# Kernel tuning notes

Hardware: AMD Instinct MI355X
Metric: run time of the kernel (lower is better)

The kernel has to match this reference:

```python
import jax, jax.numpy as jnp
import numpy as np

N = 100000
E = 1600000
D_IN, D_H, D_OUT = 128, 128, 64


def sage_conv(x, src, dst, Wl, bl, Wr, n_nodes):
    # PyG SAGEConv (aggr='mean', root_weight=True):
    # out_i = Wl @ mean_{j->i} x_j + bl + Wr @ x_i
    msg_sum = jax.ops.segment_sum(x[src], dst, num_segments=n_nodes)  # [N, d]
    deg = jax.ops.segment_sum(jnp.ones((src.shape[0],), x.dtype), dst, num_segments=n_nodes)
    agg = msg_sum / jnp.maximum(deg, 1.0)[:, None]
    return agg @ Wl + bl + x @ Wr


def setup_inputs() -> dict:
    key = jax.random.key(0)
    ks = jax.random.split(key, 12)
    x = jax.random.normal(ks[0], (N, D_IN), dtype=jnp.float32)
    edge_index = jax.random.randint(ks[1], (2, E), 0, N, dtype=jnp.int32)
    s1 = 1.0 / np.sqrt(D_IN)
    s2 = 1.0 / np.sqrt(D_H)
    return {
        "x": x,
        "edge_index": edge_index,
        "Wl1": jax.random.uniform(ks[2], (D_IN, D_H), jnp.float32, -s1, s1),
        "bl1": jax.random.uniform(ks[3], (D_H,), jnp.float32, -s1, s1),
        "Wr1": jax.random.uniform(ks[4], (D_IN, D_H), jnp.float32, -s1, s1),
        "Wl2": jax.random.uniform(ks[5], (D_H, D_H), jnp.float32, -s2, s2),
        "bl2": jax.random.uniform(ks[6], (D_H,), jnp.float32, -s2, s2),
        "Wr2": jax.random.uniform(ks[7], (D_H, D_H), jnp.float32, -s2, s2),
        "Wl3": jax.random.uniform(ks[8], (D_H, D_OUT), jnp.float32, -s2, s2),
        "bl3": jax.random.uniform(ks[9], (D_OUT,), jnp.float32, -s2, s2),
        "Wr3": jax.random.uniform(ks[10], (D_H, D_OUT), jnp.float32, -s2, s2),
    }


def reference(x, edge_index, Wl1, bl1, Wr1, Wl2, bl2, Wr2, Wl3, bl3, Wr3):
    src, dst = edge_index[0], edge_index[1]
    n = x.shape[0]
    # conv_first + relu (dropout is identity in eval mode)
    h = jax.nn.relu(sage_conv(x, src, dst, Wl1, bl1, Wr1, n))
    # conv_hidden + relu (layer_num=3 -> one hidden layer)
    h = jax.nn.relu(sage_conv(h, src, dst, Wl2, bl2, Wr2, n))
    # conv_out + L2 normalize (F.normalize, eps=1e-12)
    h = sage_conv(h, src, dst, Wl3, bl3, Wr3, n)
    norm = jnp.maximum(jnp.linalg.norm(h, axis=-1, keepdims=True), 1e-12)
    return h / norm
```

## Files before the change

kernel.cpp:

```cpp
#include <hip/hip_runtime.h>


#define BSHIFT 9
#define BNODES (1 << BSHIFT)
#define ROUND_LOG 12

typedef __attribute__((ext_vector_type(8))) short bf16x8;
typedef __attribute__((ext_vector_type(4))) float f32x4;
typedef __attribute__((ext_vector_type(8))) unsigned short u16x8;

__device__ inline float bf2f(unsigned short u) {
  unsigned v = ((unsigned)u) << 16;
  return __builtin_bit_cast(float, v);
}
__device__ inline unsigned short f2bf(float f) {
  unsigned u = __builtin_bit_cast(unsigned, f);
  u += 0x7FFF + ((u >> 16) & 1);
  return (unsigned short)(u >> 16);
}


__global__ __launch_bounds__(256) void cast_x_kernel(
    const float* __restrict__ in, unsigned short* __restrict__ out, int n8) {
  for (int i = blockIdx.x * 256 + threadIdx.x; i < n8; i += gridDim.x * 256) {
    float4 a = *(const float4*)(in + (size_t)i * 8);
    float4 b = *(const float4*)(in + (size_t)i * 8 + 4);
    u16x8 o;
    o[0] = f2bf(a.x); o[1] = f2bf(a.y); o[2] = f2bf(a.z); o[3] = f2bf(a.w);
    o[4] = f2bf(b.x); o[5] = f2bf(b.y); o[6] = f2bf(b.z); o[7] = f2bf(b.w);
    *(u16x8*)(out + (size_t)i * 8) = o;
  }
}

__global__ __launch_bounds__(256) void wtcast_kernel(
    const float* __restrict__ W, unsigned short* __restrict__ WT, int K,
    int M) {
  for (int i = blockIdx.x * 256 + threadIdx.x; i < K * M;
       i += gridDim.x * 256) {
    int k = i / M, m = i - k * M;
    WT[(size_t)m * K + k] = f2bf(W[i]);
  }
}


__global__ __launch_bounds__(256) void hist_kernel(const int* __restrict__ dst,
                                                   int E,
                                                   int* __restrict__ gcnt) {
  __shared__ int h[256];
  h[threadIdx.x] = 0;
  __syncthreads();
  for (int i = blockIdx.x * 256 + threadIdx.x; i < E; i += gridDim.x * 256)
    atomicAdd(&h[dst[i] >> BSHIFT], 1);
  __syncthreads();
  int v = h[threadIdx.x];
  if (v) atomicAdd(&gcnt[threadIdx.x], v);
}

__global__ __launch_bounds__(256) void bucket_scan_kernel(
    const int* __restrict__ gcnt, int NB, int* __restrict__ gbase,
    int* __restrict__ gcur, int* __restrict__ row_ptr, int N, int E) {
  __shared__ int sh[256];
  const int t = threadIdx.x;
  const int v = (t < NB) ? gcnt[t] : 0;
  sh[t] = v;
  __syncthreads();
  for (int d = 1; d < 256; d <<= 1) {
    int u = (t >= d) ? sh[t - d] : 0;
    __syncthreads();
    sh[t] += u;
    __syncthreads();
  }
  gbase[t] = sh[t] - v;
  gcur[t] = sh[t] - v;
  if (t == 0) row_ptr[N] = E;
}

__global__ __launch_bounds__(256) void partition_kernel(
    const int* __restrict__ src, const int* __restrict__ dst, int E,
    int* __restrict__ gcur, unsigned int* __restrict__ pairs) {
  __shared__ int lcnt[256];
  __shared__ int lbase[256];
  const int t = threadIdx.x;
  const int nRounds = (E + (1 << ROUND_LOG) - 1) >> ROUND_LOG;
  for (int r = blockIdx.x; r < nRounds; r += gridDim.x) {
    const int base = r << ROUND_LOG;
    lcnt[t] = 0;
    __syncthreads();
    int pk[16];
#pragma unroll
    for (int j = 0; j < 16; ++j) {
      int idx = base + j * 256 + t;
      pk[j] = -1;
      if (idx < E) {
        int b = dst[idx] >> BSHIFT;
        int lp = atomicAdd(&lcnt[b], 1);
        pk[j] = (b << 12) | lp;
      }
    }
    __syncthreads();
    int c = lcnt[t];
    if (c > 0) lbase[t] = atomicAdd(&gcur[t], c);
    __syncthreads();
#pragma unroll
    for (int j = 0; j < 16; ++j) {
      if (pk[j] >= 0) {
        int idx = base + j * 256 + t;
        int b = pk[j] >> 12;
        int p = lbase[b] + (pk[j] & 0xFFF);
        pairs[p] = ((unsigned)(dst[idx] & (BNODES - 1)) << 17) |
                   (unsigned)src[idx];
      }
    }
    __syncthreads();
  }
}

__global__ __launch_bounds__(256) void bucket_csr_kernel(
    const unsigned int* __restrict__ pairs, const int* __restrict__ gbase,
    const int* __restrict__ gcnt, int N, int* __restrict__ row_ptr,
    int* __restrict__ csr) {
  const int b = blockIdx.x;
  const int t = threadIdx.x;
  const int nb0 = b << BSHIFT;
  __shared__ int ldeg[BNODES];
  __shared__ int lscan[256];
  __shared__ int lcur[BNODES];
  const int base = gbase[b];
  const int cnt = gcnt[b];
  ldeg[t] = 0;
  ldeg[t + 256] = 0;
  __syncthreads();
  for (int e = t; e < cnt; e += 256)
    atomicAdd(&ldeg[pairs[base + e] >> 17], 1);
  __syncthreads();
  const int s2 = ldeg[2 * t] + ldeg[2 * t + 1];
  lscan[t] = s2;
  __syncthreads();
  for (int d = 1; d < 256; d <<= 1) {
    int u = (t >= d) ? lscan[t - d] : 0;
    __syncthreads();
    lscan[t] += u;
    __syncthreads();
  }
  const int ex = lscan[t] - s2;
  const int o0 = base + ex;
  const int o1 = o0 + ldeg[2 * t];
  const int n0 = nb0 + 2 * t;
  if (n0 < N) row_ptr[n0] = o0;
  if (n0 + 1 < N) row_ptr[n0 + 1] = o1;
  lcur[2 * t] = o0;
  lcur[2 * t + 1] = o1;
  __syncthreads();
  for (int e = t; e < cnt; e += 256) {
    unsigned int p = pairs[base + e];
    int pos = atomicAdd(&lcur[p >> 17], 1);
    csr[pos] = (int)(p & 0x1FFFF);
  }
}


__global__ __launch_bounds__(256) void gemm_dual_bf16(
    const unsigned short* __restrict__ A, const unsigned short* __restrict__ BT1,
    const unsigned short* __restrict__ BT2, const float* __restrict__ bias,
    unsigned short* __restrict__ C1, unsigned short* __restrict__ C2, int N,
    int M) {
  __shared__ unsigned short As[128][72];
  __shared__ unsigned short Bs[64][72];
  const int t = threadIdx.x;
  const int half = gridDim.x >> 1;
  int bx = blockIdx.x;
  const unsigned short* BT;
  unsigned short* C;
  const float* bs;
  if (bx < half) {
    BT = BT1; C = C1; bs = nullptr;
  } else {
    BT = BT2; C = C2; bs = bias; bx -= half;
  }
  const int rb = blockIdx.y * 128;
  const int cb = bx * 64;
  const int l = t & 63, wv = t >> 6;
  const int wr = wv >> 1, wc = wv & 1;
  const int lr = l & 15, kb = l >> 4;

  f32x4 acc[4][2];
#pragma unroll
  for (int fr = 0; fr < 4; ++fr)
#pragma unroll
    for (int fc = 0; fc < 2; ++fc) acc[fr][fc] = (f32x4)(0.f);

  const int sr = t >> 3;
  const int sc = (t & 7) * 8;

  for (int kt = 0; kt < 128; kt += 64) {
#pragma unroll
    for (int i = 0; i < 4; ++i) {
      int r = i * 32 + sr;
      int grow = rb + r;
      uint4 v = make_uint4(0, 0, 0, 0);
      if (grow < N) v = *(const uint4*)(A + (size_t)grow * 128 + kt + sc);
      *(uint4*)&As[r][sc] = v;
    }
#pragma unroll
    for (int i = 0; i < 2; ++i) {
      int r = i * 32 + sr;
      uint4 v = *(const uint4*)(BT + (size_t)(cb + r) * 128 + kt + sc);
      *(uint4*)&Bs[r][sc] = v;
    }
    __syncthreads();
#pragma unroll
    for (int ks = 0; ks < 2; ++ks) {
      bf16x8 a[4], b[2];
#pragma unroll
      for (int fr = 0; fr < 4; ++fr)
        a[fr] = *(const bf16x8*)&As[wr * 64 + fr * 16 + lr][ks * 32 + kb * 8];
#pragma unroll
      for (int fc = 0; fc < 2; ++fc)
        b[fc] = *(const bf16x8*)&Bs[wc * 32 + fc * 16 + lr][ks * 32 + kb * 8];
#pragma unroll
      for (int fr = 0; fr < 4; ++fr)
#pragma unroll
        for (int fc = 0; fc < 2; ++fc)
          acc[fr][fc] = __builtin_amdgcn_mfma_f32_16x16x32_bf16(
              a[fr], b[fc], acc[fr][fc], 0, 0, 0);
    }
    __syncthreads();
  }
#pragma unroll
  for (int fc = 0; fc < 2; ++fc) {
    int col = cb + wc * 32 + fc * 16 + lr;
    float bv = bs ? bs[col] : 0.f;
#pragma unroll
    for (int fr = 0; fr < 4; ++fr) {
      int row0 = rb + wr * 64 + fr * 16 + kb * 4;
#pragma unroll
      for (int j = 0; j < 4; ++j) {
        int row = row0 + j;
        if (row < N) C[(size_t)row * M + col] = f2bf(acc[fr][fc][j] + bv);
      }
    }
  }
}


__global__ __launch_bounds__(256) void agg_relu_bf16_128(
    const unsigned short* __restrict__ z, const unsigned short* __restrict__ w,
    const int* __restrict__ row_ptr, const int* __restrict__ csr,
    unsigned short* __restrict__ out, int N) {
  const int g = threadIdx.x >> 4;
  const int lane = threadIdx.x & 15;
  const int node = blockIdx.x * 16 + g;
  if (node >= N) return;
  const int s = row_ptr[node];
  const int e = row_ptr[node + 1];
  float a0[8] = {0, 0, 0, 0, 0, 0, 0, 0};
  float a1[8] = {0, 0, 0, 0, 0, 0, 0, 0};
  int i = s;
  for (; i + 1 < e; i += 2) {
    u16x8 v0 = *(const u16x8*)(z + (size_t)csr[i] * 128 + lane * 8);
    u16x8 v1 = *(const u16x8*)(z + (size_t)csr[i + 1] * 128 + lane * 8);
#pragma unroll
    for (int j = 0; j < 8; ++j) {
      a0[j] += bf2f(v0[j]);
      a1[j] += bf2f(v1[j]);
    }
  }
  if (i < e) {
    u16x8 v0 = *(const u16x8*)(z + (size_t)csr[i] * 128 + lane * 8);
#pragma unroll
    for (int j = 0; j < 8; ++j) a0[j] += bf2f(v0[j]);
  }
  const int d = e - s;
  const float inv = 1.0f / (float)(d > 0 ? d : 1);
  u16x8 wv = *(const u16x8*)(w + (size_t)node * 128 + lane * 8);
  u16x8 o;
#pragma unroll
  for (int j = 0; j < 8; ++j)
    o[j] = f2bf(fmaxf(fmaf(a0[j] + a1[j], inv, bf2f(wv[j])), 0.f));
  *(u16x8*)(out + (size_t)node * 128 + lane * 8) = o;
}

__global__ __launch_bounds__(256) void agg_norm_bf16_64(
    const unsigned short* __restrict__ z, const unsigned short* __restrict__ w,
    const int* __restrict__ row_ptr, const int* __restrict__ csr,
    float* __restrict__ out, int N) {
  const int g = threadIdx.x >> 3;
  const int lane = threadIdx.x & 7;
  const int node = blockIdx.x * 32 + g;
  if (node >= N) return;
  const int s = row_ptr[node];
  const int e = row_ptr[node + 1];
  float a0[8] = {0, 0, 0, 0, 0, 0, 0, 0};
  float a1[8] = {0, 0, 0, 0, 0, 0, 0, 0};
  int i = s;
  for (; i + 1 < e; i += 2) {
    u16x8 v0 = *(const u16x8*)(z + (size_t)csr[i] * 64 + lane * 8);
    u16x8 v1 = *(const u16x8*)(z + (size_t)csr[i + 1] * 64 + lane * 8);
#pragma unroll
    for (int j = 0; j < 8; ++j) {
      a0[j] += bf2f(v0[j]);
      a1[j] += bf2f(v1[j]);
    }
  }
  if (i < e) {
    u16x8 v0 = *(const u16x8*)(z + (size_t)csr[i] * 64 + lane * 8);
#pragma unroll
    for (int j = 0; j < 8; ++j) a0[j] += bf2f(v0[j]);
  }
  const int d = e - s;
  const float inv = 1.0f / (float)(d > 0 ? d : 1);
  u16x8 wv = *(const u16x8*)(w + (size_t)node * 64 + lane * 8);
  float v[8];
  float n2 = 0.f;
#pragma unroll
  for (int j = 0; j < 8; ++j) {
    v[j] = fmaf(a0[j] + a1[j], inv, bf2f(wv[j]));
    n2 = fmaf(v[j], v[j], n2);
  }
  n2 += __shfl_xor(n2, 1);
  n2 += __shfl_xor(n2, 2);
  n2 += __shfl_xor(n2, 4);
  const float invn = 1.0f / fmaxf(sqrtf(n2), 1e-12f);
  float* op = out + (size_t)node * 64 + lane * 8;
  float4 o0 = make_float4(v[0] * invn, v[1] * invn, v[2] * invn, v[3] * invn);
  float4 o1 = make_float4(v[4] * invn, v[5] * invn, v[6] * invn, v[7] * invn);
  *(float4*)op = o0;
  *(float4*)(op + 4) = o1;
}


extern "C" void kernel_launch(void* const* d_in, const int* in_sizes, int n_in,
                              void* d_out, int out_size, void* d_ws,
                              size_t ws_size, hipStream_t stream) {
  const float* x   = (const float*)d_in[0];
  const int*   ei  = (const int*)d_in[1];
  const float* Wl1 = (const float*)d_in[2];
  const float* bl1 = (const float*)d_in[3];
  const float* Wr1 = (const float*)d_in[4];
  const float* Wl2 = (const float*)d_in[5];
  const float* bl2 = (const float*)d_in[6];
  const float* Wr2 = (const float*)d_in[7];
  const float* Wl3 = (const float*)d_in[8];
  const float* bl3 = (const float*)d_in[9];
  const float* Wr3 = (const float*)d_in[10];

  const int N = in_sizes[0] / 128;
  const int E = in_sizes[1] / 2;
  const int* src = ei;
  const int* dst = ei + E;
  const int NB = (N + BNODES - 1) >> BSHIFT;

  char* ws = (char*)d_ws;
  size_t off = 0;
  auto take = [&](size_t bytes) -> char* {
    char* p = ws + off;
    off += (bytes + 255) & ~(size_t)255;
    return p;
  };
  unsigned short* xb   = (unsigned short*)take((size_t)N * 128 * 2);
  unsigned short* h    = (unsigned short*)take((size_t)N * 128 * 2);
  unsigned short* z    = (unsigned short*)take((size_t)N * 128 * 2);
  unsigned short* w    = (unsigned short*)take((size_t)N * 128 * 2);
  unsigned short* WT[6];
  for (int i = 0; i < 6; ++i) WT[i] = (unsigned short*)take(128 * 128 * 2);
  int*          row_ptr = (int*)take((size_t)(N + 1) * 4);
  int*          csr     = (int*)take((size_t)E * 4);
  unsigned int* pairs   = (unsigned int*)take((size_t)E * 4);
  int*          gcnt    = (int*)take(256 * 4);
  int*          gbase   = (int*)take(256 * 4);
  int*          gcur    = (int*)take(256 * 4);
  (void)ws_size;

  hipMemsetAsync(gcnt, 0, 256 * 4, stream);
  hist_kernel<<<1024, 256, 0, stream>>>(dst, E, gcnt);
  bucket_scan_kernel<<<1, 256, 0, stream>>>(gcnt, NB, gbase, gcur, row_ptr, N, E);
  const int nRounds = (E + (1 << ROUND_LOG) - 1) >> ROUND_LOG;
  partition_kernel<<<nRounds, 256, 0, stream>>>(src, dst, E, gcur, pairs);
  bucket_csr_kernel<<<NB, 256, 0, stream>>>(pairs, gbase, gcnt, N, row_ptr, csr);

  cast_x_kernel<<<2048, 256, 0, stream>>>(x, xb, N * 16);
  wtcast_kernel<<<64, 256, 0, stream>>>(Wl1, WT[0], 128, 128);
  wtcast_kernel<<<64, 256, 0, stream>>>(Wr1, WT[1], 128, 128);
  wtcast_kernel<<<64, 256, 0, stream>>>(Wl2, WT[2], 128, 128);
  wtcast_kernel<<<64, 256, 0, stream>>>(Wr2, WT[3], 128, 128);
  wtcast_kernel<<<32, 256, 0, stream>>>(Wl3, WT[4], 128, 64);
  wtcast_kernel<<<32, 256, 0, stream>>>(Wr3, WT[5], 128, 64);

  const dim3 blk(256);
  const int rowBlocks = (N + 127) / 128;
  const dim3 gd2(4, rowBlocks);
  const dim3 gd1(2, rowBlocks);
  const int aggB128 = (N + 15) / 16;
  const int aggB64  = (N + 31) / 32;

  gemm_dual_bf16<<<gd2, blk, 0, stream>>>(xb, WT[0], WT[1], bl1, z, w, N, 128);
  agg_relu_bf16_128<<<aggB128, blk, 0, stream>>>(z, w, row_ptr, csr, h, N);
  gemm_dual_bf16<<<gd2, blk, 0, stream>>>(h, WT[2], WT[3], bl2, z, w, N, 128);
  agg_relu_bf16_128<<<aggB128, blk, 0, stream>>>(z, w, row_ptr, csr, h, N);
  gemm_dual_bf16<<<gd1, blk, 0, stream>>>(h, WT[4], WT[5], bl3, z, w, N, 64);
  agg_norm_bf16_64<<<aggB64, blk, 0, stream>>>(z, w, row_ptr, csr,
                                               (float*)d_out, N);
}
```

Measured before the change: 458.2 us.

## Slice Z/W into 16-column feature planes for cache-friendly gather aggregation

The first two layers' GEMM outputs are written in a sliced layout: eight planes of 16 columns each. The aggregation kernel then handles one slice per block, so each gather of a neighbour row touches 32 bytes, and the per-slice working set (N×32B) can stay in L2 across edges. The dual GEMM now computes both Wl and Wr products in a single block, with both weight matrices loaded as one concatenated B tile, and weight casting is merged into three launches. In exchange, each gather uses smaller 8-byte loads, the edge list is re-read once per slice, and the GEMM stores become scattered.

```diff
diff --git a/kernel.cpp b/kernel.cpp
--- a/kernel.cpp
+++ b/kernel.cpp
@@ -32,13 +32,15 @@
   }
 }
 
-__global__ __launch_bounds__(256) void wtcast_kernel(
-    const float* __restrict__ W, unsigned short* __restrict__ WT, int K,
-    int M) {
-  for (int i = blockIdx.x * 256 + threadIdx.x; i < K * M;
+__global__ __launch_bounds__(256) void wtcast2_kernel(
+    const float* __restrict__ Wl, const float* __restrict__ Wr,
+    unsigned short* __restrict__ BT, int K, int M) {
+  const int total = 2 * M * K;
+  for (int i = blockIdx.x * 256 + threadIdx.x; i < total;
        i += gridDim.x * 256) {
-    int k = i / M, m = i - k * M;
-    WT[(size_t)m * K + k] = f2bf(W[i]);
+    int r = i / K, k = i - r * K;
+    float v = (r < M) ? Wl[(size_t)k * M + r] : Wr[(size_t)k * M + (r - M)];
+    BT[i] = f2bf(v);
   }
 }
 
@@ -159,35 +161,26 @@
 }
 
 
-__global__ __launch_bounds__(256) void gemm_dual_bf16(
-    const unsigned short* __restrict__ A, const unsigned short* __restrict__ BT1,
-    const unsigned short* __restrict__ BT2, const float* __restrict__ bias,
-    unsigned short* __restrict__ C1, unsigned short* __restrict__ C2, int N,
-    int M) {
+template <int MH, bool SLICED>
+__global__ __launch_bounds__(256) void gemm_dual(
+    const unsigned short* __restrict__ A, const unsigned short* __restrict__ BT,
+    const float* __restrict__ bias, unsigned short* __restrict__ Zs,
+    unsigned short* __restrict__ Ws, int N) {
+  constexpr int MT = 2 * MH;
+  constexpr int F = MH / 16;
   __shared__ unsigned short As[128][72];
-  __shared__ unsigned short Bs[64][72];
+  __shared__ unsigned short Bs[MT][72];
   const int t = threadIdx.x;
-  const int half = gridDim.x >> 1;
-  int bx = blockIdx.x;
-  const unsigned short* BT;
-  unsigned short* C;
-  const float* bs;
-  if (bx < half) {
-    BT = BT1; C = C1; bs = nullptr;
-  } else {
-    BT = BT2; C = C2; bs = bias; bx -= half;
-  }
-  const int rb = blockIdx.y * 128;
-  const int cb = bx * 64;
+  const int rb = blockIdx.x * 128;
   const int l = t & 63, wv = t >> 6;
   const int wr = wv >> 1, wc = wv & 1;
   const int lr = l & 15, kb = l >> 4;
 
-  f32x4 acc[4][2];
+  f32x4 acc[4][F];
 #pragma unroll
   for (int fr = 0; fr < 4; ++fr)
 #pragma unroll
-    for (int fc = 0; fc < 2; ++fc) acc[fr][fc] = (f32x4)(0.f);
+    for (int fc = 0; fc < F; ++fc) acc[fr][fc] = (f32x4)(0.f);
 
   const int sr = t >> 3;
   const int sc = (t & 7) * 8;
@@ -202,83 +195,100 @@
       *(uint4*)&As[r][sc] = v;
     }
 #pragma unroll
-    for (int i = 0; i < 2; ++i) {
+    for (int i = 0; i < MT / 32; ++i) {
       int r = i * 32 + sr;
-      uint4 v = *(const uint4*)(BT + (size_t)(cb + r) * 128 + kt + sc);
+      uint4 v = *(const uint4*)(BT + (size_t)r * 128 + kt + sc);
       *(uint4*)&Bs[r][sc] = v;
     }
     __syncthreads();
 #pragma unroll
     for (int ks = 0; ks < 2; ++ks) {
-      bf16x8 a[4], b[2];
+      bf16x8 a[4], b[F];
 #pragma unroll
       for (int fr = 0; fr < 4; ++fr)
         a[fr] = *(const bf16x8*)&As[wr * 64 + fr * 16 + lr][ks * 32 + kb * 8];
 #pragma unroll
-      for (int fc = 0; fc < 2; ++fc)
-        b[fc] = *(const bf16x8*)&Bs[wc * 32 + fc * 16 + lr][ks * 32 + kb * 8];
+      for (int fc = 0; fc < F; ++fc)
+        b[fc] = *(const bf16x8*)&Bs[wc * MH + fc * 16 + lr][ks * 32 + kb * 8];
 #pragma unroll
       for (int fr = 0; fr < 4; ++fr)
 #pragma unroll
-        for (int fc = 0; fc < 2; ++fc)
+        for (int fc = 0; fc < F; ++fc)
           acc[fr][fc] = __builtin_amdgcn_mfma_f32_16x16x32_bf16(
               a[fr], b[fc], acc[fr][fc], 0, 0, 0);
     }
     __syncthreads();
   }
-#pragma unroll
-  for (int fc = 0; fc < 2; ++fc) {
-    int col = cb + wc * 32 + fc * 16 + lr;
-    float bv = bs ? bs[col] : 0.f;
+  unsigned short* Cb = wc ? Ws : Zs;
+#pragma unroll
+  for (int fc = 0; fc < F; ++fc) {
+    const int cm = fc * 16 + lr;
+    const float bv = wc ? bias[cm] : 0.f;
 #pragma unroll
     for (int fr = 0; fr < 4; ++fr) {
-      int row0 = rb + wr * 64 + fr * 16 + kb * 4;
+      const int row0 = rb + wr * 64 + fr * 16 + kb * 4;
 #pragma unroll
       for (int j = 0; j < 4; ++j) {
-        int row = row0 + j;
-        if (row < N) C[(size_t)row * M + col] = f2bf(acc[fr][fc][j] + bv);
+        const int row = row0 + j;
+        if (row < N) {
+          size_t idx = SLICED ? ((size_t)(fc * N + row) * 16 + lr)
+                              : ((size_t)row * MH + cm);
+          Cb[idx] = f2bf(acc[fr][fc][j] + bv);
+        }
       }
     }
   }
 }
 
 
-__global__ __launch_bounds__(256) void agg_relu_bf16_128(
-    const unsigned short* __restrict__ z, const unsigned short* __restrict__ w,
+__global__ __launch_bounds__(256) void agg_relu_sliced(
+    const unsigned short* __restrict__ Zs, const unsigned short* __restrict__ Ws,
     const int* __restrict__ row_ptr, const int* __restrict__ csr,
     unsigned short* __restrict__ out, int N) {
-  const int g = threadIdx.x >> 4;
-  const int lane = threadIdx.x & 15;
-  const int node = blockIdx.x * 16 + g;
+  const int s = blockIdx.x & 7;
+  const int grp = blockIdx.x >> 3;
+  const int node = grp * 64 + (threadIdx.x >> 2);
+  const int l4 = threadIdx.x & 3;
   if (node >= N) return;
-  const int s = row_ptr[node];
+  const int sB = row_ptr[node];
   const int e = row_ptr[node + 1];
-  float a0[8] = {0, 0, 0, 0, 0, 0, 0, 0};
-  float a1[8] = {0, 0, 0, 0, 0, 0, 0, 0};
-  int i = s;
+  const unsigned short* zb = Zs + (size_t)s * N * 16 + l4 * 4;
+  float a0[4] = {0, 0, 0, 0}, a1[4] = {0, 0, 0, 0};
+  int i = sB;
   for (; i + 1 < e; i += 2) {
-    u16x8 v0 = *(const u16x8*)(z + (size_t)csr[i] * 128 + lane * 8);
-    u16x8 v1 = *(const u16x8*)(z + (size_t)csr[i + 1] * 128 + lane * 8);
-#pragma unroll
-    for (int j = 0; j < 8; ++j) {
-      a0[j] += bf2f(v0[j]);
-      a1[j] += bf2f(v1[j]);
-    }
+    uint2 v0 = *(const uint2*)(zb + (size_t)csr[i] * 16);
+    uint2 v1 = *(const uint2*)(zb + (size_t)csr[i + 1] * 16);
+    a0[0] += bf2f((unsigned short)v0.x);
+    a0[1] += bf2f((unsigned short)(v0.x >> 16));
+    a0[2] += bf2f((unsigned short)v0.y);
+    a0[3] += bf2f((unsigned short)(v0.y >> 16));
+    a1[0] += bf2f((unsigned short)v1.x);
+    a1[1] += bf2f((unsigned short)(v1.x >> 16));
+    a1[2] += bf2f((unsigned short)v1.y);
+    a1[3] += bf2f((unsigned short)(v1.y >> 16));
   }
   if (i < e) {
-    u16x8 v0 = *(const u16x8*)(z + (size_t)csr[i] * 128 + lane * 8);
-#pragma unroll
-    for (int j = 0; j < 8; ++j) a0[j] += bf2f(v0[j]);
-  }
-  const int d = e - s;
+    uint2 v0 = *(const uint2*)(zb + (size_t)csr[i] * 16);
+    a0[0] += bf2f((unsigned short)v0.x);
+    a0[1] += bf2f((unsigned short)(v0.x >> 16));
+    a0[2] += bf2f((unsigned short)v0.y);
+    a0[3] += bf2f((unsigned short)(v0.y >> 16));
+  }
+  const int d = e - sB;
   const float inv = 1.0f / (float)(d > 0 ? d : 1);
-  u16x8 wv = *(const u16x8*)(w + (size_t)node * 128 + lane * 8);
-  u16x8 o;
-#pragma unroll
-  for (int j = 0; j < 8; ++j)
-    o[j] = f2bf(fmaxf(fmaf(a0[j] + a1[j], inv, bf2f(wv[j])), 0.f));
-  *(u16x8*)(out + (size_t)node * 128 + lane * 8) = o;
-}
+  uint2 wv = *(const uint2*)(Ws + ((size_t)s * N + node) * 16 + l4 * 4);
+  float r0 = fmaxf(fmaf(a0[0] + a1[0], inv, bf2f((unsigned short)wv.x)), 0.f);
+  float r1 =
+      fmaxf(fmaf(a0[1] + a1[1], inv, bf2f((unsigned short)(wv.x >> 16))), 0.f);
+  float r2 = fmaxf(fmaf(a0[2] + a1[2], inv, bf2f((unsigned short)wv.y)), 0.f);
+  float r3 =
+      fmaxf(fmaf(a0[3] + a1[3], inv, bf2f((unsigned short)(wv.y >> 16))), 0.f);
+  uint2 o;
+  o.x = (unsigned)f2bf(r0) | ((unsigned)f2bf(r1) << 16);
+  o.y = (unsigned)f2bf(r2) | ((unsigned)f2bf(r3) << 16);
+  *(uint2*)(out + (size_t)node * 128 + s * 16 + l4 * 4) = o;
+}
+
 
 __global__ __launch_bounds__(256) void agg_norm_bf16_64(
     const unsigned short* __restrict__ z, const unsigned short* __restrict__ w,
@@ -361,8 +371,9 @@
   unsigned short* h    = (unsigned short*)take((size_t)N * 128 * 2);
   unsigned short* z    = (unsigned short*)take((size_t)N * 128 * 2);
   unsigned short* w    = (unsigned short*)take((size_t)N * 128 * 2);
-  unsigned short* WT[6];
-  for (int i = 0; i < 6; ++i) WT[i] = (unsigned short*)take(128 * 128 * 2);
+  unsigned short* BT1  = (unsigned short*)take(256 * 128 * 2);
+  unsigned short* BT2  = (unsigned short*)take(256 * 128 * 2);
+  unsigned short* BT3  = (unsigned short*)take(128 * 128 * 2);
   int*          row_ptr = (int*)take((size_t)(N + 1) * 4);
   int*          csr     = (int*)take((size_t)E * 4);
   unsigned int* pairs   = (unsigned int*)take((size_t)E * 4);
@@ -379,25 +390,20 @@
   bucket_csr_kernel<<<NB, 256, 0, stream>>>(pairs, gbase, gcnt, N, row_ptr, csr);
 
   cast_x_kernel<<<2048, 256, 0, stream>>>(x, xb, N * 16);
-  wtcast_kernel<<<64, 256, 0, stream>>>(Wl1, WT[0], 128, 128);
-  wtcast_kernel<<<64, 256, 0, stream>>>(Wr1, WT[1], 128, 128);
-  wtcast_kernel<<<64, 256, 0, stream>>>(Wl2, WT[2], 128, 128);
-  wtcast_kernel<<<64, 256, 0, stream>>>(Wr2, WT[3], 128, 128);
-  wtcast_kernel<<<32, 256, 0, stream>>>(Wl3, WT[4], 128, 64);
-  wtcast_kernel<<<32, 256, 0, stream>>>(Wr3, WT[5], 128, 64);
+  wtcast2_kernel<<<128, 256, 0, stream>>>(Wl1, Wr1, BT1, 128, 128);
+  wtcast2_kernel<<<128, 256, 0, stream>>>(Wl2, Wr2, BT2, 128, 128);
+  wtcast2_kernel<<<64, 256, 0, stream>>>(Wl3, Wr3, BT3, 128, 64);
 
   const dim3 blk(256);
   const int rowBlocks = (N + 127) / 128;
-  const dim3 gd2(4, rowBlocks);
-  const dim3 gd1(2, rowBlocks);
-  const int aggB128 = (N + 15) / 16;
-  const int aggB64  = (N + 31) / 32;
-
-  gemm_dual_bf16<<<gd2, blk, 0, stream>>>(xb, WT[0], WT[1], bl1, z, w, N, 128);
-  agg_relu_bf16_128<<<aggB128, blk, 0, stream>>>(z, w, row_ptr, csr, h, N);
-  gemm_dual_bf16<<<gd2, blk, 0, stream>>>(h, WT[2], WT[3], bl2, z, w, N, 128);
-  agg_relu_bf16_128<<<aggB128, blk, 0, stream>>>(z, w, row_ptr, csr, h, N);
-  gemm_dual_bf16<<<gd1, blk, 0, stream>>>(h, WT[4], WT[5], bl3, z, w, N, 64);
+  const int aggSliced = ((N + 63) / 64) * 8;
+  const int aggB64 = (N + 31) / 32;
+
+  gemm_dual<128, true><<<rowBlocks, blk, 0, stream>>>(xb, BT1, bl1, z, w, N);
+  agg_relu_sliced<<<aggSliced, blk, 0, stream>>>(z, w, row_ptr, csr, h, N);
+  gemm_dual<128, true><<<rowBlocks, blk, 0, stream>>>(h, BT2, bl2, z, w, N);
+  agg_relu_sliced<<<aggSliced, blk, 0, stream>>>(z, w, row_ptr, csr, h, N);
+  gemm_dual<64, false><<<rowBlocks, blk, 0, stream>>>(h, BT3, bl3, z, w, N);
   agg_norm_bf16_64<<<aggB64, blk, 0, stream>>>(z, w, row_ptr, csr,
                                                (float*)d_out, N);
 }
```

Result: slower. 620.4 us (+35.4%).

## Fuse x cast into first GEMM, merge weight casts, widen GEMM tiles, unroll gather

Applied to the files above, without the earlier changes.

The first layer's GEMM now reads fp32 x directly and converts it to bf16 while staging into shared memory, which removes the separate cast kernel and its bf16 round trip through memory. The six weight-transpose kernels become one launch that packs the Wl and Wr weights of each layer into a single stacked buffer. Each GEMM block now covers the full output width (128 or 64 columns), so the A tile is loaded once per matrix instead of twice, at the cost of more accumulator registers. The 128-wide aggregation loop is unrolled by four with independent accumulators to keep more gathers in flight.

```diff
diff --git a/kernel.cpp b/kernel.cpp
--- a/kernel.cpp
+++ b/kernel.cpp
@@ -20,25 +20,31 @@
 }
 
 
-__global__ __launch_bounds__(256) void cast_x_kernel(
-    const float* __restrict__ in, unsigned short* __restrict__ out, int n8) {
-  for (int i = blockIdx.x * 256 + threadIdx.x; i < n8; i += gridDim.x * 256) {
-    float4 a = *(const float4*)(in + (size_t)i * 8);
-    float4 b = *(const float4*)(in + (size_t)i * 8 + 4);
-    u16x8 o;
-    o[0] = f2bf(a.x); o[1] = f2bf(a.y); o[2] = f2bf(a.z); o[3] = f2bf(a.w);
-    o[4] = f2bf(b.x); o[5] = f2bf(b.y); o[6] = f2bf(b.z); o[7] = f2bf(b.w);
-    *(u16x8*)(out + (size_t)i * 8) = o;
-  }
-}
-
-__global__ __launch_bounds__(256) void wtcast_kernel(
-    const float* __restrict__ W, unsigned short* __restrict__ WT, int K,
-    int M) {
-  for (int i = blockIdx.x * 256 + threadIdx.x; i < K * M;
+__global__ __launch_bounds__(256) void wtcast_all_kernel(
+    const float* __restrict__ Wl1, const float* __restrict__ Wr1,
+    const float* __restrict__ Wl2, const float* __restrict__ Wr2,
+    const float* __restrict__ Wl3, const float* __restrict__ Wr3,
+    unsigned short* __restrict__ BT1, unsigned short* __restrict__ BT2,
+    unsigned short* __restrict__ BT3) {
+  const int K = 128;
+  const int n12 = 2 * 128 * K;
+  const int n3 = 2 * 64 * K;
+  const int total = 2 * n12 + n3;
+  for (int i = blockIdx.x * 256 + threadIdx.x; i < total;
        i += gridDim.x * 256) {
-    int k = i / M, m = i - k * M;
-    WT[(size_t)m * K + k] = f2bf(W[i]);
+    const float *Wl, *Wr;
+    unsigned short* BT;
+    int j, M;
+    if (i < n12) {
+      Wl = Wl1; Wr = Wr1; BT = BT1; j = i; M = 128;
+    } else if (i < 2 * n12) {
+      Wl = Wl2; Wr = Wr2; BT = BT2; j = i - n12; M = 128;
+    } else {
+      Wl = Wl3; Wr = Wr3; BT = BT3; j = i - 2 * n12; M = 64;
+    }
+    int r = j / K, k = j - r * K;
+    float v = (r < M) ? Wl[(size_t)k * M + r] : Wr[(size_t)k * M + (r - M)];
+    BT[j] = f2bf(v);
   }
 }
 
@@ -159,35 +165,28 @@
 }
 
 
-__global__ __launch_bounds__(256) void gemm_dual_bf16(
-    const unsigned short* __restrict__ A, const unsigned short* __restrict__ BT1,
-    const unsigned short* __restrict__ BT2, const float* __restrict__ bias,
-    unsigned short* __restrict__ C1, unsigned short* __restrict__ C2, int N,
-    int M) {
+template <int MH, bool AFP32>
+__global__ __launch_bounds__(256) void gemm_dual(
+    const void* __restrict__ Av, const unsigned short* __restrict__ BT,
+    const float* __restrict__ bias, unsigned short* __restrict__ Z,
+    unsigned short* __restrict__ W, int N) {
+  constexpr int F = MH / 32;
   __shared__ unsigned short As[128][72];
-  __shared__ unsigned short Bs[64][72];
+  __shared__ unsigned short Bs[MH][72];
   const int t = threadIdx.x;
-  const int half = gridDim.x >> 1;
-  int bx = blockIdx.x;
-  const unsigned short* BT;
-  unsigned short* C;
-  const float* bs;
-  if (bx < half) {
-    BT = BT1; C = C1; bs = nullptr;
-  } else {
-    BT = BT2; C = C2; bs = bias; bx -= half;
-  }
+  const int mat = blockIdx.x;
+  const unsigned short* BTm = BT + (size_t)mat * MH * 128;
+  unsigned short* C = mat ? W : Z;
   const int rb = blockIdx.y * 128;
-  const int cb = bx * 64;
   const int l = t & 63, wv = t >> 6;
   const int wr = wv >> 1, wc = wv & 1;
   const int lr = l & 15, kb = l >> 4;
 
-  f32x4 acc[4][2];
+  f32x4 acc[4][F];
 #pragma unroll
   for (int fr = 0; fr < 4; ++fr)
 #pragma unroll
-    for (int fc = 0; fc < 2; ++fc) acc[fr][fc] = (f32x4)(0.f);
+    for (int fc = 0; fc < F; ++fc) acc[fr][fc] = (f32x4)(0.f);
 
   const int sr = t >> 3;
   const int sc = (t & 7) * 8;
@@ -197,46 +196,63 @@
     for (int i = 0; i < 4; ++i) {
       int r = i * 32 + sr;
       int grow = rb + r;
-      uint4 v = make_uint4(0, 0, 0, 0);
-      if (grow < N) v = *(const uint4*)(A + (size_t)grow * 128 + kt + sc);
-      *(uint4*)&As[r][sc] = v;
-    }
-#pragma unroll
-    for (int i = 0; i < 2; ++i) {
+      if constexpr (AFP32) {
+        const float* Af = (const float*)Av;
+        float4 v0 = make_float4(0.f, 0.f, 0.f, 0.f);
+        float4 v1 = make_float4(0.f, 0.f, 0.f, 0.f);
+        if (grow < N) {
+          v0 = *(const float4*)(Af + (size_t)grow * 128 + kt + sc);
+          v1 = *(const float4*)(Af + (size_t)grow * 128 + kt + sc + 4);
+        }
+        u16x8 o;
+        o[0] = f2bf(v0.x); o[1] = f2bf(v0.y); o[2] = f2bf(v0.z);
+        o[3] = f2bf(v0.w); o[4] = f2bf(v1.x); o[5] = f2bf(v1.y);
+        o[6] = f2bf(v1.z); o[7] = f2bf(v1.w);
+        *(u16x8*)&As[r][sc] = o;
+      } else {
+        const unsigned short* Ab = (const unsigned short*)Av;
+        uint4 v = make_uint4(0, 0, 0, 0);
+        if (grow < N) v = *(const uint4*)(Ab + (size_t)grow * 128 + kt + sc);
+        *(uint4*)&As[r][sc] = v;
+      }
+    }
+#pragma unroll
+    for (int i = 0; i < MH / 32; ++i) {
       int r = i * 32 + sr;
-      uint4 v = *(const uint4*)(BT + (size_t)(cb + r) * 128 + kt + sc);
+      uint4 v = *(const uint4*)(BTm + (size_t)r * 128 + kt + sc);
       *(uint4*)&Bs[r][sc] = v;
     }
     __syncthreads();
 #pragma unroll
     for (int ks = 0; ks < 2; ++ks) {
-      bf16x8 a[4], b[2];
+      bf16x8 a[4], b[F];
 #pragma unroll
       for (int fr = 0; fr < 4; ++fr)
         a[fr] = *(const bf16x8*)&As[wr * 64 + fr * 16 + lr][ks * 32 + kb * 8];
 #pragma unroll
-      for (int fc = 0; fc < 2; ++fc)
-        b[fc] = *(const bf16x8*)&Bs[wc * 32 + fc * 16 + lr][ks * 32 + kb * 8];
+      for (int fc = 0; fc < F; ++fc)
+        b[fc] =
+            *(const bf16x8*)&Bs[wc * (MH / 2) + fc * 16 + lr][ks * 32 + kb * 8];
 #pragma unroll
       for (int fr = 0; fr < 4; ++fr)
 #pragma unroll
-        for (int fc = 0; fc < 2; ++fc)
+        for (int fc = 0; fc < F; ++fc)
           acc[fr][fc] = __builtin_amdgcn_mfma_f32_16x16x32_bf16(
               a[fr], b[fc], acc[fr][fc], 0, 0, 0);
     }
     __syncthreads();
   }
 #pragma unroll
-  for (int fc = 0; fc < 2; ++fc) {
-    int col = cb + wc * 32 + fc * 16 + lr;
-    float bv = bs ? bs[col] : 0.f;
+  for (int fc = 0; fc < F; ++fc) {
+    const int cm = wc * (MH / 2) + fc * 16 + lr;
+    const float bv = mat ? bias[cm] : 0.f;
 #pragma unroll
     for (int fr = 0; fr < 4; ++fr) {
-      int row0 = rb + wr * 64 + fr * 16 + kb * 4;
+      const int row0 = rb + wr * 64 + fr * 16 + kb * 4;
 #pragma unroll
       for (int j = 0; j < 4; ++j) {
-        int row = row0 + j;
-        if (row < N) C[(size_t)row * M + col] = f2bf(acc[fr][fc][j] + bv);
+        const int row = row0 + j;
+        if (row < N) C[(size_t)row * MH + cm] = f2bf(acc[fr][fc][j] + bv);
       }
     }
   }
@@ -255,17 +271,24 @@
   const int e = row_ptr[node + 1];
   float a0[8] = {0, 0, 0, 0, 0, 0, 0, 0};
   float a1[8] = {0, 0, 0, 0, 0, 0, 0, 0};
+  float a2[8] = {0, 0, 0, 0, 0, 0, 0, 0};
+  float a3[8] = {0, 0, 0, 0, 0, 0, 0, 0};
   int i = s;
-  for (; i + 1 < e; i += 2) {
-    u16x8 v0 = *(const u16x8*)(z + (size_t)csr[i] * 128 + lane * 8);
-    u16x8 v1 = *(const u16x8*)(z + (size_t)csr[i + 1] * 128 + lane * 8);
+  for (; i + 3 < e; i += 4) {
+    int s0 = csr[i], s1 = csr[i + 1], s2 = csr[i + 2], s3 = csr[i + 3];
+    u16x8 v0 = *(const u16x8*)(z + (size_t)s0 * 128 + lane * 8);
+    u16x8 v1 = *(const u16x8*)(z + (size_t)s1 * 128 + lane * 8);
+    u16x8 v2 = *(const u16x8*)(z + (size_t)s2 * 128 + lane * 8);
+    u16x8 v3 = *(const u16x8*)(z + (size_t)s3 * 128 + lane * 8);
 #pragma unroll
     for (int j = 0; j < 8; ++j) {
       a0[j] += bf2f(v0[j]);
       a1[j] += bf2f(v1[j]);
-    }
-  }
-  if (i < e) {
+      a2[j] += bf2f(v2[j]);
+      a3[j] += bf2f(v3[j]);
+    }
+  }
+  for (; i < e; ++i) {
     u16x8 v0 = *(const u16x8*)(z + (size_t)csr[i] * 128 + lane * 8);
 #pragma unroll
     for (int j = 0; j < 8; ++j) a0[j] += bf2f(v0[j]);
@@ -275,8 +298,10 @@
   u16x8 wv = *(const u16x8*)(w + (size_t)node * 128 + lane * 8);
   u16x8 o;
 #pragma unroll
-  for (int j = 0; j < 8; ++j)
-    o[j] = f2bf(fmaxf(fmaf(a0[j] + a1[j], inv, bf2f(wv[j])), 0.f));
+  for (int j = 0; j < 8; ++j) {
+    float sum = (a0[j] + a1[j]) + (a2[j] + a3[j]);
+    o[j] = f2bf(fmaxf(fmaf(sum, inv, bf2f(wv[j])), 0.f));
+  }
   *(u16x8*)(out + (size_t)node * 128 + lane * 8) = o;
 }
 
@@ -357,12 +382,12 @@
     off += (bytes + 255) & ~(size_t)255;
     return p;
   };
-  unsigned short* xb   = (unsigned short*)take((size_t)N * 128 * 2);
   unsigned short* h    = (unsigned short*)take((size_t)N * 128 * 2);
   unsigned short* z    = (unsigned short*)take((size_t)N * 128 * 2);
   unsigned short* w    = (unsigned short*)take((size_t)N * 128 * 2);
-  unsigned short* WT[6];
-  for (int i = 0; i < 6; ++i) WT[i] = (unsigned short*)take(128 * 128 * 2);
+  unsigned short* BT1  = (unsigned short*)take(256 * 128 * 2);
+  unsigned short* BT2  = (unsigned short*)take(256 * 128 * 2);
+  unsigned short* BT3  = (unsigned short*)take(128 * 128 * 2);
   int*          row_ptr = (int*)take((size_t)(N + 1) * 4);
   int*          csr     = (int*)take((size_t)E * 4);
   unsigned int* pairs   = (unsigned int*)take((size_t)E * 4);
@@ -378,26 +403,20 @@
   partition_kernel<<<nRounds, 256, 0, stream>>>(src, dst, E, gcur, pairs);
   bucket_csr_kernel<<<NB, 256, 0, stream>>>(pairs, gbase, gcnt, N, row_ptr, csr);
 
-  cast_x_kernel<<<2048, 256, 0, stream>>>(x, xb, N * 16);
-  wtcast_kernel<<<64, 256, 0, stream>>>(Wl1, WT[0], 128, 128);
-  wtcast_kernel<<<64, 256, 0, stream>>>(Wr1, WT[1], 128, 128);
-  wtcast_kernel<<<64, 256, 0, stream>>>(Wl2, WT[2], 128, 128);
-  wtcast_kernel<<<64, 256, 0, stream>>>(Wr2, WT[3], 128, 128);
-  wtcast_kernel<<<32, 256, 0, stream>>>(Wl3, WT[4], 128, 64);
-  wtcast_kernel<<<32, 256, 0, stream>>>(Wr3, WT[5], 128, 64);
+  wtcast_all_kernel<<<320, 256, 0, stream>>>(Wl1, Wr1, Wl2, Wr2, Wl3, Wr3, BT1,
+                                             BT2, BT3);
 
   const dim3 blk(256);
   const int rowBlocks = (N + 127) / 128;
-  const dim3 gd2(4, rowBlocks);
-  const dim3 gd1(2, rowBlocks);
+  const dim3 gg(2, rowBlocks);
   const int aggB128 = (N + 15) / 16;
   const int aggB64  = (N + 31) / 32;
 
-  gemm_dual_bf16<<<gd2, blk, 0, stream>>>(xb, WT[0], WT[1], bl1, z, w, N, 128);
+  gemm_dual<128, true><<<gg, blk, 0, stream>>>(x, BT1, bl1, z, w, N);
   agg_relu_bf16_128<<<aggB128, blk, 0, stream>>>(z, w, row_ptr, csr, h, N);
-  gemm_dual_bf16<<<gd2, blk, 0, stream>>>(h, WT[2], WT[3], bl2, z, w, N, 128);
+  gemm_dual<128, false><<<gg, blk, 0, stream>>>(h, BT2, bl2, z, w, N);
   agg_relu_bf16_128<<<aggB128, blk, 0, stream>>>(z, w, row_ptr, csr, h, N);
-  gemm_dual_bf16<<<gd1, blk, 0, stream>>>(h, WT[4], WT[5], bl3, z, w, N, 64);
+  gemm_dual<64, false><<<gg, blk, 0, stream>>>(h, BT3, bl3, z, w, N);
   agg_norm_bf16_64<<<aggB64, blk, 0, stream>>>(z, w, row_ptr, csr,
                                                (float*)d_out, N);
 }
```

After: 460.4 us. Within noise of the previous version (+0.5%).
